# Kernel optimization log

Hardware: AMD Instinct MI355X
Metric: run time of the kernel (lower is better)

The kernel has to match this reference:

```python
import jax, jax.numpy as jnp
import numpy as np
from jax import lax

WINDOW_SIZE = 11
SIGMA = 1.5
DATA_RANGE = 1.0
C1 = (0.01 * DATA_RANGE) ** 2
C2 = (0.03 * DATA_RANGE) ** 2


def _gauss_1d():
    half = WINDOW_SIZE // 2
    xs = np.arange(WINDOW_SIZE, dtype=np.float32)
    g = np.exp(-((xs - half) ** 2) / (2.0 * SIGMA ** 2)).astype(np.float32)
    g = g / g.sum()
    return jnp.asarray(g)


def _blur3d(v, g1d):
    """Depthwise 3D Gaussian blur via three separable 1D convs (same math as
    conv3d with the outer-product window, padding=window_size//2)."""
    C = v.shape[1]
    pad = WINDOW_SIZE // 2
    dn = lax.conv_dimension_numbers(v.shape, (C, 1, WINDOW_SIZE, 1, 1),
                                    ('NCDHW', 'OIDHW', 'NCDHW'))
    for axis in range(3):  # D, H, W
        kshape = [1, 1, 1]
        kshape[axis] = WINDOW_SIZE
        kern = jnp.broadcast_to(g1d.reshape(kshape)[None, None], (C, 1, *kshape))
        padding = [(0, 0)] * 3
        padding[axis] = (pad, pad)
        v = lax.conv_general_dilated(v, kern, window_strides=(1, 1, 1),
                                     padding=padding, dimension_numbers=dn,
                                     feature_group_count=C)
    return v


def setup_inputs() -> dict:
    key = jax.random.key(0)
    k1, k2 = jax.random.split(key)
    shape = (2, 1, 160, 160, 160)
    x = jax.random.uniform(k1, shape, dtype=jnp.float32)
    y = jax.random.uniform(k2, shape, dtype=jnp.float32)
    return {"x": x, "y": y}


def reference(x, y):
    g1d = _gauss_1d()
    mu_x = _blur3d(x, g1d)
    mu_y = _blur3d(y, g1d)
    mu_x_sq = mu_x * mu_x
    mu_y_sq = mu_y * mu_y
    mu_xy = mu_x * mu_y
    sigma_x_sq = _blur3d(x * x, g1d) - mu_x_sq
    sigma_y_sq = _blur3d(y * y, g1d) - mu_y_sq
    sigma_xy = _blur3d(x * y, g1d) - mu_xy
    ssim_map = ((2.0 * mu_xy + C1) * (2.0 * sigma_xy + C2)) / (
        (mu_x_sq + mu_y_sq + C1) * (sigma_x_sq + sigma_y_sq + C2))
    return ssim_map.mean()  # size_average=True
```

## Files before the change

### kernel.cpp

```cpp
#include <hip/hip_runtime.h>
#include <cmath>

#define WS   11
#define PAD  5
#define NX   160
#define NB   2
#define TH   20
#define TW   32
#define SH   (TH + 2*PAD)
#define SW   (TW + 2*PAD)
#define NF   5
#define DCHUNK 40

static const long long PLANE = (long long)NB * NX * NX * NX;

struct GaussW { float g[WS]; };

__constant__ const float C1v = 1.0e-4f;
__constant__ const float C2v = 9.0e-4f;

__global__ __launch_bounds__(256) void k_wh(const float* __restrict__ x,
                                            const float* __restrict__ y,
                                            float* __restrict__ A,
                                            GaussW gw) {
    __shared__ float sx[SH][SW];
    __shared__ float sy[SH][SW];
    __shared__ float mid[NF][SH][TW];

    const int tid = threadIdx.x;
    const int b  = blockIdx.z / NX;
    const int d  = blockIdx.z % NX;
    const int h0 = blockIdx.y * TH;
    const int w0 = blockIdx.x * TW;
    const long long slice = (long long)(b * NX + d) * (NX * NX);

    for (int idx = tid; idx < SH * SW; idx += 256) {
        const int r = idx / SW, c = idx % SW;
        const int gh = h0 - PAD + r;
        const int gww = w0 - PAD + c;
        float xv = 0.f, yv = 0.f;
        if (gh >= 0 && gh < NX && gww >= 0 && gww < NX) {
            const long long o = slice + (long long)gh * NX + gww;
            xv = x[o]; yv = y[o];
        }
        sx[r][c] = xv;
        sy[r][c] = yv;
    }
    __syncthreads();

    for (int idx = tid; idx < SH * TW; idx += 256) {
        const int r = idx >> 5, c = idx & 31;
        float a0 = 0.f, a1 = 0.f, a2 = 0.f, a3 = 0.f, a4 = 0.f;
        #pragma unroll
        for (int k = 0; k < WS; ++k) {
            const float gk = gw.g[k];
            const float xv = sx[r][c + k];
            const float yv = sy[r][c + k];
            a0 += gk * xv;
            a1 += gk * yv;
            a2 += gk * xv * xv;
            a3 += gk * yv * yv;
            a4 += gk * xv * yv;
        }
        mid[0][r][c] = a0; mid[1][r][c] = a1; mid[2][r][c] = a2;
        mid[3][r][c] = a3; mid[4][r][c] = a4;
    }
    __syncthreads();

    for (int idx = tid; idx < TH * TW; idx += 256) {
        const int r = idx >> 5, c = idx & 31;
        float a0 = 0.f, a1 = 0.f, a2 = 0.f, a3 = 0.f, a4 = 0.f;
        #pragma unroll
        for (int k = 0; k < WS; ++k) {
            const float gk = gw.g[k];
            a0 += gk * mid[0][r + k][c];
            a1 += gk * mid[1][r + k][c];
            a2 += gk * mid[2][r + k][c];
            a3 += gk * mid[3][r + k][c];
            a4 += gk * mid[4][r + k][c];
        }
        const long long o = slice + (long long)(h0 + r) * NX + (w0 + c);
        A[o]             = a0;
        A[PLANE + o]     = a1;
        A[2 * PLANE + o] = a2;
        A[3 * PLANE + o] = a3;
        A[4 * PLANE + o] = a4;
    }
}

__global__ __launch_bounds__(256) void k_d(const float* __restrict__ A,
                                           float* __restrict__ partial,
                                           GaussW gw) {
    const int tid = threadIdx.x;
    const long long gidx = (long long)blockIdx.x * 256 + tid;
    const int NCOL = NB * NX * NX;
    const int chunk = (int)(gidx / NCOL);
    const int col   = (int)(gidx % NCOL);
    const int b  = col / (NX * NX);
    const int hw = col % (NX * NX);
    const long long base = (long long)b * (NX * NX * NX) + hw;
    const int d0 = chunk * DCHUNK;

    float win[NF][WS];
    #pragma unroll
    for (int i = 0; i < WS; ++i) {
        const int di = d0 - PAD + i;
        const bool ok = (di >= 0 && di < NX);
        const long long o = base + (long long)(ok ? di : 0) * (NX * NX);
        #pragma unroll
        for (int f = 0; f < NF; ++f)
            win[f][i] = ok ? A[(long long)f * PLANE + o] : 0.f;
    }

    float acc = 0.f;
    for (int dd = 0; dd < DCHUNK; ++dd) {
        float m[NF];
        #pragma unroll
        for (int f = 0; f < NF; ++f) {
            float s = 0.f;
            #pragma unroll
            for (int i = 0; i < WS; ++i) s += gw.g[i] * win[f][i];
            m[f] = s;
        }
        const float mux = m[0], muy = m[1];
        const float mux2 = mux * mux, muy2 = muy * muy, muxy = mux * muy;
        const float sx_  = m[2] - mux2;
        const float sy_  = m[3] - muy2;
        const float sxy = m[4] - muxy;
        const float num = (2.f * muxy + C1v) * (2.f * sxy + C2v);
        const float den = (mux2 + muy2 + C1v) * (sx_ + sy_ + C2v);
        acc += num / den;

        const int dn = d0 + dd + PAD + 1;
        const bool ok = (dn < NX);
        const long long o = base + (long long)(ok ? dn : 0) * (NX * NX);
        #pragma unroll
        for (int f = 0; f < NF; ++f) {
            #pragma unroll
            for (int i = 0; i < WS - 1; ++i) win[f][i] = win[f][i + 1];
            win[f][WS - 1] = ok ? A[(long long)f * PLANE + o] : 0.f;
        }
    }

    for (int off = 32; off > 0; off >>= 1) acc += __shfl_down(acc, off, 64);
    __shared__ float wsum[4];
    if ((tid & 63) == 0) wsum[tid >> 6] = acc;
    __syncthreads();
    if (tid == 0) partial[blockIdx.x] = wsum[0] + wsum[1] + wsum[2] + wsum[3];
}

__global__ __launch_bounds__(256) void k_red(const float* __restrict__ partial,
                                             int n, float* __restrict__ out) {
    double s = 0.0;
    for (int i = threadIdx.x; i < n; i += 256) s += (double)partial[i];
    __shared__ double sd[256];
    sd[threadIdx.x] = s;
    __syncthreads();
    for (int st = 128; st > 0; st >>= 1) {
        if (threadIdx.x < st) sd[threadIdx.x] += sd[threadIdx.x + st];
        __syncthreads();
    }
    if (threadIdx.x == 0)
        out[0] = (float)(sd[0] / (double)((long long)NB * NX * NX * NX));
}

extern "C" void kernel_launch(void* const* d_in, const int* in_sizes, int n_in,
                              void* d_out, int out_size, void* d_ws, size_t ws_size,
                              hipStream_t stream) {
    const float* x = (const float*)d_in[0];
    const float* y = (const float*)d_in[1];
    float* A = (float*)d_ws;
    float* partial = (float*)((char*)d_ws + (size_t)NF * PLANE * sizeof(float));

    GaussW gw;
    {
        float tmp[WS]; float s = 0.f;
        for (int i = 0; i < WS; ++i) {
            const double e = exp(-(double)((i - PAD) * (i - PAD)) / 4.5);
            tmp[i] = (float)e; s += tmp[i];
        }
        for (int i = 0; i < WS; ++i) gw.g[i] = tmp[i] / s;
    }

    dim3 g1(NX / TW, NX / TH, NB * NX);
    k_wh<<<g1, 256, 0, stream>>>(x, y, A, gw);

    const int nblk2 = (NB * NX * NX * (NX / DCHUNK)) / 256;
    k_d<<<nblk2, 256, 0, stream>>>(A, partial, gw);

    k_red<<<1, 256, 0, stream>>>(partial, nblk2, (float*)d_out);
}
```

Baseline: 117.0 us.

## Register-block W/H blur passes with vectorized LDS loads and 32-bit indexing

Reworks the fused W/H blur kernel so each thread computes 4 adjacent W outputs from a float4-loaded 16-element register window, and 2 adjacent H rows per thread, reusing loaded values instead of re-reading shared memory per tap. The global tile load uses float2 vector loads with an offset-aligned, padded shared row. Tile height drops to 16 so work maps exactly onto 256 threads, and all index math moves from 64-bit to 32-bit. This cuts LDS traffic and address arithmetic, at the cost of more halo overhead per tile and more registers.

```diff
diff --git a/kernel.cpp b/kernel.cpp
--- a/kernel.cpp
+++ b/kernel.cpp
@@ -2,17 +2,16 @@
 #include <cmath>
 
 #define WS   11
-#define PAD  5
 #define NX   160
 #define NB   2
-#define TH   20
+#define TH   16
 #define TW   32
-#define SH   (TH + 2*PAD)
-#define SW   (TW + 2*PAD)
+#define SH   (TH + 10)
+#define SWP  44
 #define NF   5
 #define DCHUNK 40
 
-static const long long PLANE = (long long)NB * NX * NX * NX;
+#define PLANE_I 8192000
 
 struct GaussW { float g[WS]; };
 
@@ -23,8 +22,8 @@
                                             const float* __restrict__ y,
                                             float* __restrict__ A,
                                             GaussW gw) {
-    __shared__ float sx[SH][SW];
-    __shared__ float sy[SH][SW];
+    __shared__ float sx[SH][SWP];
+    __shared__ float sy[SH][SWP];
     __shared__ float mid[NF][SH][TW];
 
     const int tid = threadIdx.x;
@@ -32,59 +31,82 @@
     const int d  = blockIdx.z % NX;
     const int h0 = blockIdx.y * TH;
     const int w0 = blockIdx.x * TW;
-    const long long slice = (long long)(b * NX + d) * (NX * NX);
-
-    for (int idx = tid; idx < SH * SW; idx += 256) {
-        const int r = idx / SW, c = idx % SW;
-        const int gh = h0 - PAD + r;
-        const int gww = w0 - PAD + c;
-        float xv = 0.f, yv = 0.f;
-        if (gh >= 0 && gh < NX && gww >= 0 && gww < NX) {
-            const long long o = slice + (long long)gh * NX + gww;
-            xv = x[o]; yv = y[o];
-        }
-        sx[r][c] = xv;
-        sy[r][c] = yv;
-    }
-    __syncthreads();
-
-    for (int idx = tid; idx < SH * TW; idx += 256) {
-        const int r = idx >> 5, c = idx & 31;
-        float a0 = 0.f, a1 = 0.f, a2 = 0.f, a3 = 0.f, a4 = 0.f;
+    const int slice = (b * NX + d) * (NX * NX);
+
+    for (int t = tid; t < SH * 22; t += 256) {
+        const int r = t / 22, c2 = t % 22;
+        const int gh = h0 - 5 + r;
+        const int gwc = w0 - 6 + 2 * c2;
+        float2 xv = make_float2(0.f, 0.f), yv = make_float2(0.f, 0.f);
+        if ((unsigned)gh < (unsigned)NX) {
+            const int o = slice + gh * NX + gwc;
+            if (gwc >= 0 && gwc + 1 < NX) {
+                xv = *(const float2*)(x + o);
+                yv = *(const float2*)(y + o);
+            } else {
+                if ((unsigned)gwc < (unsigned)NX)       { xv.x = x[o];     yv.x = y[o]; }
+                if ((unsigned)(gwc + 1) < (unsigned)NX) { xv.y = x[o + 1]; yv.y = y[o + 1]; }
+            }
+        }
+        *(float2*)&sx[r][2 * c2] = xv;
+        *(float2*)&sy[r][2 * c2] = yv;
+    }
+    __syncthreads();
+
+    if (tid < SH * 8) {
+        const int r  = tid >> 3;
+        const int c4 = (tid & 7) << 2;
+        const float4* px = (const float4*)&sx[r][c4];
+        const float4* py = (const float4*)&sy[r][c4];
+        const float4 X0 = px[0], X1 = px[1], X2 = px[2], X3 = px[3];
+        const float4 Y0 = py[0], Y1 = py[1], Y2 = py[2], Y3 = py[3];
+        const float wx[16] = {X0.x,X0.y,X0.z,X0.w, X1.x,X1.y,X1.z,X1.w,
+                              X2.x,X2.y,X2.z,X2.w, X3.x,X3.y,X3.z,X3.w};
+        const float wy[16] = {Y0.x,Y0.y,Y0.z,Y0.w, Y1.x,Y1.y,Y1.z,Y1.w,
+                              Y2.x,Y2.y,Y2.z,Y2.w, Y3.x,Y3.y,Y3.z,Y3.w};
+        float a0[4] = {0,0,0,0}, a1[4] = {0,0,0,0}, a2[4] = {0,0,0,0},
+              a3[4] = {0,0,0,0}, a4[4] = {0,0,0,0};
         #pragma unroll
         for (int k = 0; k < WS; ++k) {
             const float gk = gw.g[k];
-            const float xv = sx[r][c + k];
-            const float yv = sy[r][c + k];
-            a0 += gk * xv;
-            a1 += gk * yv;
-            a2 += gk * xv * xv;
-            a3 += gk * yv * yv;
-            a4 += gk * xv * yv;
-        }
-        mid[0][r][c] = a0; mid[1][r][c] = a1; mid[2][r][c] = a2;
-        mid[3][r][c] = a3; mid[4][r][c] = a4;
-    }
-    __syncthreads();
-
-    for (int idx = tid; idx < TH * TW; idx += 256) {
-        const int r = idx >> 5, c = idx & 31;
-        float a0 = 0.f, a1 = 0.f, a2 = 0.f, a3 = 0.f, a4 = 0.f;
-        #pragma unroll
-        for (int k = 0; k < WS; ++k) {
-            const float gk = gw.g[k];
-            a0 += gk * mid[0][r + k][c];
-            a1 += gk * mid[1][r + k][c];
-            a2 += gk * mid[2][r + k][c];
-            a3 += gk * mid[3][r + k][c];
-            a4 += gk * mid[4][r + k][c];
-        }
-        const long long o = slice + (long long)(h0 + r) * NX + (w0 + c);
-        A[o]             = a0;
-        A[PLANE + o]     = a1;
-        A[2 * PLANE + o] = a2;
-        A[3 * PLANE + o] = a3;
-        A[4 * PLANE + o] = a4;
+            #pragma unroll
+            for (int j = 0; j < 4; ++j) {
+                const float xv = wx[j + k + 1];
+                const float yv = wy[j + k + 1];
+                const float t0 = gk * xv;
+                const float t1 = gk * yv;
+                a0[j] += t0;      a1[j] += t1;
+                a2[j] += t0 * xv; a3[j] += t1 * yv; a4[j] += t0 * yv;
+            }
+        }
+        *(float4*)&mid[0][r][c4] = make_float4(a0[0], a0[1], a0[2], a0[3]);
+        *(float4*)&mid[1][r][c4] = make_float4(a1[0], a1[1], a1[2], a1[3]);
+        *(float4*)&mid[2][r][c4] = make_float4(a2[0], a2[1], a2[2], a2[3]);
+        *(float4*)&mid[3][r][c4] = make_float4(a3[0], a3[1], a3[2], a3[3]);
+        *(float4*)&mid[4][r][c4] = make_float4(a4[0], a4[1], a4[2], a4[3]);
+    }
+    __syncthreads();
+
+    {
+        const int rg = tid >> 5;
+        const int c  = tid & 31;
+        const int r0 = rg * 2;
+        float b0[NF] = {0,0,0,0,0}, b1[NF] = {0,0,0,0,0};
+        #pragma unroll
+        for (int k = 0; k < 12; ++k) {
+            #pragma unroll
+            for (int f = 0; f < NF; ++f) {
+                const float v = mid[f][r0 + k][c];
+                if (k <= 10) b0[f] += gw.g[k] * v;
+                if (k >= 1)  b1[f] += gw.g[k - 1] * v;
+            }
+        }
+        const int aofs = slice + (h0 + r0) * NX + w0 + c;
+        #pragma unroll
+        for (int f = 0; f < NF; ++f) {
+            A[f * PLANE_I + aofs]      = b0[f];
+            A[f * PLANE_I + aofs + NX] = b1[f];
+        }
     }
 }
 
@@ -98,18 +120,18 @@
     const int col   = (int)(gidx % NCOL);
     const int b  = col / (NX * NX);
     const int hw = col % (NX * NX);
-    const long long base = (long long)b * (NX * NX * NX) + hw;
+    const int base = b * (NX * NX * NX) + hw;
     const int d0 = chunk * DCHUNK;
 
     float win[NF][WS];
     #pragma unroll
     for (int i = 0; i < WS; ++i) {
-        const int di = d0 - PAD + i;
+        const int di = d0 - 5 + i;
         const bool ok = (di >= 0 && di < NX);
-        const long long o = base + (long long)(ok ? di : 0) * (NX * NX);
+        const int o = base + (ok ? di : 0) * (NX * NX);
         #pragma unroll
         for (int f = 0; f < NF; ++f)
-            win[f][i] = ok ? A[(long long)f * PLANE + o] : 0.f;
+            win[f][i] = ok ? A[f * PLANE_I + o] : 0.f;
     }
 
     float acc = 0.f;
@@ -124,21 +146,21 @@
         }
         const float mux = m[0], muy = m[1];
         const float mux2 = mux * mux, muy2 = muy * muy, muxy = mux * muy;
-        const float sx_  = m[2] - mux2;
-        const float sy_  = m[3] - muy2;
+        const float sx_ = m[2] - mux2;
+        const float sy_ = m[3] - muy2;
         const float sxy = m[4] - muxy;
         const float num = (2.f * muxy + C1v) * (2.f * sxy + C2v);
         const float den = (mux2 + muy2 + C1v) * (sx_ + sy_ + C2v);
         acc += num / den;
 
-        const int dn = d0 + dd + PAD + 1;
+        const int dn = d0 + dd + 6;
         const bool ok = (dn < NX);
-        const long long o = base + (long long)(ok ? dn : 0) * (NX * NX);
+        const int o = base + (ok ? dn : 0) * (NX * NX);
         #pragma unroll
         for (int f = 0; f < NF; ++f) {
             #pragma unroll
             for (int i = 0; i < WS - 1; ++i) win[f][i] = win[f][i + 1];
-            win[f][WS - 1] = ok ? A[(long long)f * PLANE + o] : 0.f;
+            win[f][WS - 1] = ok ? A[f * PLANE_I + o] : 0.f;
         }
     }
 
@@ -170,13 +192,13 @@
     const float* x = (const float*)d_in[0];
     const float* y = (const float*)d_in[1];
     float* A = (float*)d_ws;
-    float* partial = (float*)((char*)d_ws + (size_t)NF * PLANE * sizeof(float));
+    float* partial = (float*)((char*)d_ws + (size_t)NF * PLANE_I * sizeof(float));
 
     GaussW gw;
     {
         float tmp[WS]; float s = 0.f;
         for (int i = 0; i < WS; ++i) {
-            const double e = exp(-(double)((i - PAD) * (i - PAD)) / 4.5);
+            const double e = exp(-(double)((i - 5) * (i - 5)) / 4.5);
             tmp[i] = (float)e; s += tmp[i];
         }
         for (int i = 0; i < WS; ++i) gw.g[i] = tmp[i] / s;
```

Result: no change. 117.1 us (+0.0%).
